# Kernel tuning notes

Hardware: AMD Instinct MI355X
Metric: run time of the kernel (lower is better)

Reference implementation:

```python
import jax, jax.numpy as jnp
import numpy as np

IN_DIM = 768
ATT_DIM = 512
N_HEADS = 8
HEAD_DIM = ATT_DIM // N_HEADS


def setup_inputs() -> dict:
    key = jax.random.key(0)
    k1, k2, k3 = jax.random.split(key, 3)
    X = jax.random.normal(k1, (4, 2048, IN_DIM), dtype=jnp.float32)
    # qkv linear (no bias): weight [3*att_dim, in_dim], torch convention y = x W^T
    W_qkv = jax.random.normal(k2, (3 * ATT_DIM, IN_DIM), dtype=jnp.float32) * (1.0 / np.sqrt(IN_DIM))
    W_out = jax.random.normal(k3, (IN_DIM, ATT_DIM), dtype=jnp.float32) * (1.0 / np.sqrt(ATT_DIM))
    b_out = jnp.zeros((IN_DIM,), dtype=jnp.float32)
    return {"X": X, "W_qkv": W_qkv, "W_out": W_out, "b_out": b_out}


def reference(X, W_qkv, W_out, b_out):
    b, n, _ = X.shape
    QKV = jnp.einsum('bnf,cf->bnc', X, W_qkv)  # [b, n, 3*att_dim]
    # rearrange 'b n (p h d) -> p b h n d'
    QKV = QKV.reshape(b, n, 3, N_HEADS, HEAD_DIM).transpose(2, 0, 3, 1, 4)
    Q, K, V = QKV[0], QKV[1], QKV[2]  # each [b, h, n, d]
    scores = jnp.einsum('bhid,bhjd->bhij', Q, K) / np.sqrt(HEAD_DIM)
    A = jax.nn.softmax(scores, axis=-1)  # dropout p=0 -> identity
    Y = jnp.einsum('bhij,bhjd->bhid', A, V)
    Y = Y.transpose(0, 2, 1, 3).reshape(b, n, ATT_DIM)  # 'b h n d -> b n (h d)'
    return jnp.einsum('bna,oa->bno', Y, W_out) + b_out
```

## Files before the change

kernel.cpp:

```cpp
#include <hip/hip_runtime.h>

typedef __bf16 bf16;
typedef unsigned int u32;
typedef __attribute__((ext_vector_type(8))) __bf16 bf16x8;
typedef __attribute__((ext_vector_type(4))) __bf16 bf16x4;
typedef __attribute__((ext_vector_type(4))) float floatx4;

#define IN_DIM  768
#define ATT_DIM 512
#define NH      8
#define HD      64
#define BATCH   4
#define SEQ     2048
#define M_TOT   (BATCH*SEQ)
#define QKV_N   (3*ATT_DIM)

#define QSCALE 0.18033688011112042f

__device__ __forceinline__ void cp16(void* lds, const void* g) {
    __builtin_amdgcn_global_load_lds((const __attribute__((address_space(1))) u32*)g,
                                     (__attribute__((address_space(3))) u32*)lds, 16, 0, 0);
}
__device__ __forceinline__ const bf16* swz(const bf16* b, int row, int chunk) {
    return b + row * 64 + (((chunk) ^ (row & 7)) << 3);
}
__device__ __forceinline__ const bf16* swz128(const bf16* b, int row, int chunk) {
    return b + row * 128 + (((chunk) ^ (row & 15)) << 3);
}

#define N8_X  (M_TOT * IN_DIM / 8)
#define N8_WQ (QKV_N * IN_DIM / 8)
#define N8_WO (IN_DIM * ATT_DIM / 8)
#define N8_ALL (N8_X + N8_WQ + N8_WO)

__global__ __launch_bounds__(256) void cvt_all(const float* __restrict__ X,
                                               const float* __restrict__ Wq,
                                               const float* __restrict__ Wo,
                                               bf16* __restrict__ Xb,
                                               bf16* __restrict__ Wqb,
                                               bf16* __restrict__ Wob) {
    int i = blockIdx.x * 256 + threadIdx.x;
    const float* s; bf16* d; int off;
    if (i < N8_X)            { s = X;  d = Xb;  off = i; }
    else if (i < N8_X+N8_WQ) { s = Wq; d = Wqb; off = i - N8_X; }
    else                     { s = Wo; d = Wob; off = i - N8_X - N8_WQ; }
    const float4 a = ((const float4*)s)[2*off];
    const float4 b = ((const float4*)s)[2*off+1];
    bf16x8 o = {(bf16)a.x,(bf16)a.y,(bf16)a.z,(bf16)a.w,
                (bf16)b.x,(bf16)b.y,(bf16)b.z,(bf16)b.w};
    ((bf16x8*)d)[off] = o;
}

__global__ __launch_bounds__(256) void qkv_gemm(const bf16* __restrict__ Xb,
                                                const bf16* __restrict__ Wb,
                                                bf16* __restrict__ Q,
                                                bf16* __restrict__ Kv,
                                                bf16* __restrict__ VT) {
    __shared__ __align__(16) char smraw[34816];
    bf16* As = (bf16*)smraw;
    bf16* Bs = (bf16*)(smraw + 16384);

    const int tid  = threadIdx.x;
    const int bm0  = blockIdx.y * 128;
    const int bn0  = blockIdx.x * 128;
    const int wave = tid >> 6, lane = tid & 63;
    const int quad = lane >> 4, l15 = lane & 15;
    const int wm = (wave >> 1) * 64, wn = (wave & 1) * 64;
    const int r8 = lane >> 3, cc = (lane & 7) ^ r8;

    const bf16* ag = Xb + (size_t)(bm0 + wave * 32 + r8) * IN_DIM + cc * 8;
    const bf16* bg = Wb + (size_t)(bn0 + wave * 32 + r8) * IN_DIM + cc * 8;

    floatx4 acc[4][4];
#pragma unroll
    for (int i = 0; i < 4; ++i)
#pragma unroll
        for (int j = 0; j < 4; ++j) acc[i][j] = (floatx4){0.f, 0.f, 0.f, 0.f};

    for (int kt = 0; kt < IN_DIM / 64; ++kt) {
        __syncthreads();
#pragma unroll
        for (int it = 0; it < 4; ++it) {
            cp16(&As[(wave * 32 + it * 8) * 64], ag + it * (8 * IN_DIM) + kt * 64);
            cp16(&Bs[(wave * 32 + it * 8) * 64], bg + it * (8 * IN_DIM) + kt * 64);
        }
        __syncthreads();

        bf16x8 af[2][4], bfr[2][4];
#pragma unroll
        for (int kh = 0; kh < 2; ++kh)
#pragma unroll
            for (int i = 0; i < 4; ++i) {
                af[kh][i]  = *(const bf16x8*)swz(As, wm + i * 16 + l15, kh * 4 + quad);
                bfr[kh][i] = *(const bf16x8*)swz(Bs, wn + i * 16 + l15, kh * 4 + quad);
            }
#pragma unroll
        for (int kh = 0; kh < 2; ++kh)
#pragma unroll
            for (int i = 0; i < 4; ++i)
#pragma unroll
                for (int j = 0; j < 4; ++j)
                    acc[i][j] = __builtin_amdgcn_mfma_f32_16x16x32_bf16(af[kh][i], bfr[kh][j], acc[i][j], 0, 0, 0);
    }

    const int b = bm0 >> 11, nbase = bm0 & 2047;

    if (bn0 < 1024) {
#pragma unroll
        for (int i = 0; i < 4; ++i)
#pragma unroll
            for (int j = 0; j < 4; ++j)
#pragma unroll
                for (int r = 0; r < 4; ++r) {
                    const int row = bm0 + wm + i * 16 + quad * 4 + r;
                    const int col = bn0 + wn + j * 16 + l15;
                    const float v = acc[i][j][r];
                    const int rem = col & 511;
                    const int h = rem >> 6, d = rem & 63;
                    const int n = row & 2047;
                    const size_t idx = (((size_t)((row >> 11) * NH + h)) * SEQ + n) * HD + d;
                    if (col < 512) Q[idx]  = (bf16)(v * QSCALE);
                    else           Kv[idx] = (bf16)v;
                }
    } else {
        __syncthreads();
        bf16 (*Ts)[136] = (bf16(*)[136])smraw;
#pragma unroll
        for (int i = 0; i < 4; ++i)
#pragma unroll
            for (int j = 0; j < 4; ++j) {
                bf16x4 pk = {(bf16)acc[i][j][0], (bf16)acc[i][j][1],
                             (bf16)acc[i][j][2], (bf16)acc[i][j][3]};
                *(bf16x4*)&Ts[wn + j * 16 + l15][wm + i * 16 + quad * 4] = pk;
            }
        __syncthreads();
        const int cb = bn0 - 1024;
#pragma unroll
        for (int t2 = 0; t2 < 8; ++t2) {
            const int id = tid + t2 * 256;
            const int c = id >> 4, nc = (id & 15) * 8;
            const int col = cb + c;
            const int h = col >> 6, d = col & 63;
            *(bf16x8*)&VT[(((size_t)(b * NH + h)) * HD + d) * SEQ + nbase + nc] =
                *(const bf16x8*)&Ts[c][nc];
        }
    }
}

__global__ __launch_bounds__(256, 2) void attn(const bf16* __restrict__ Q,
                                               const bf16* __restrict__ K,
                                               const bf16* __restrict__ VT,
                                               bf16* __restrict__ Y) {
    __shared__ bf16 Ks[2][128 * 64];
    __shared__ bf16 VTs[2][64 * 128];
    __shared__ bf16 Ps[4][2][16 * 64];

    const int tid  = threadIdx.x;
    const int wave = tid >> 6, lane = tid & 63;
    const int quad = lane >> 4, l15 = lane & 15;
    const int bh = blockIdx.x;
    const int q0 = blockIdx.y * 128;
    const bf16* Qg = Q  + (size_t)bh * SEQ * HD;
    const bf16* Kg = K  + (size_t)bh * SEQ * HD;
    const bf16* Vg = VT + (size_t)bh * HD * SEQ;

    const int r8 = lane >> 3, cc = (lane & 7) ^ r8;
    const int r4 = lane >> 4;

    bf16x8 aq[2][2];
#pragma unroll
    for (int g = 0; g < 2; ++g) {
        const size_t qrow = (size_t)(q0 + wave * 32 + g * 16 + l15) * 64;
        aq[g][0] = *(const bf16x8*)&Qg[qrow + quad * 8];
        aq[g][1] = *(const bf16x8*)&Qg[qrow + 32 + quad * 8];
    }

    const bf16* kgw = Kg + (size_t)(wave * 32 + r8) * 64 + cc * 8;
    float l[2] = {0.f, 0.f};
    floatx4 o[2][4];
#pragma unroll
    for (int g = 0; g < 2; ++g)
#pragma unroll
        for (int db = 0; db < 4; ++db) o[g][db] = (floatx4){0.f, 0.f, 0.f, 0.f};

#pragma unroll
    for (int it = 0; it < 4; ++it)
        cp16(&Ks[0][(wave * 32 + it * 8) * 64], kgw + (size_t)it * 8 * 64);
#pragma unroll
    for (int it = 0; it < 4; ++it) {
        const int vrow = wave * 16 + it * 4 + r4;
        const int vcc = (lane & 15) ^ (vrow & 15);
        cp16(&VTs[0][(wave * 16 + it * 4) * 128],
             Vg + (size_t)vrow * 2048 + vcc * 8);
    }

    for (int kt = 0; kt < SEQ / 128; ++kt) {
        const int cur = kt & 1, nb = cur ^ 1;
        __syncthreads();
        if (kt < SEQ / 128 - 1) {
#pragma unroll
            for (int it = 0; it < 4; ++it)
                cp16(&Ks[nb][(wave * 32 + it * 8) * 64],
                     kgw + (size_t)(kt + 1) * 128 * 64 + (size_t)it * 8 * 64);
#pragma unroll
            for (int it = 0; it < 4; ++it) {
                const int vrow = wave * 16 + it * 4 + r4;
                const int vcc = (lane & 15) ^ (vrow & 15);
                cp16(&VTs[nb][(wave * 16 + it * 4) * 128],
                     Vg + (size_t)vrow * 2048 + (kt + 1) * 128 + vcc * 8);
            }
        }

#pragma unroll
        for (int s = 0; s < 2; ++s) {
#pragma unroll
            for (int t = 0; t < 4; ++t) {
                const int kr = s * 64 + t * 16 + l15;
                const bf16x8 k0 = *(const bf16x8*)swz(Ks[cur], kr, quad);
                const bf16x8 k1 = *(const bf16x8*)swz(Ks[cur], kr, 4 + quad);
                const int c = t * 2 + (quad >> 1);
                const int poff = l15 * 64 + ((c ^ (l15 & 7)) << 3) + ((quad & 1) << 2);
#pragma unroll
                for (int g = 0; g < 2; ++g) {
                    floatx4 z = (floatx4){0.f, 0.f, 0.f, 0.f};
                    z = __builtin_amdgcn_mfma_f32_16x16x32_bf16(k0, aq[g][0], z, 0, 0, 0);
                    z = __builtin_amdgcn_mfma_f32_16x16x32_bf16(k1, aq[g][1], z, 0, 0, 0);
                    const float p0 = __builtin_amdgcn_exp2f(z[0]);
                    const float p1 = __builtin_amdgcn_exp2f(z[1]);
                    const float p2 = __builtin_amdgcn_exp2f(z[2]);
                    const float p3 = __builtin_amdgcn_exp2f(z[3]);
                    l[g] += (p0 + p1) + (p2 + p3);
                    bf16x4 pk = {(bf16)p0, (bf16)p1, (bf16)p2, (bf16)p3};
                    *(bf16x4*)&Ps[wave][g][poff] = pk;
                }
            }
            bf16x8 pa[2][2];
#pragma unroll
            for (int g = 0; g < 2; ++g) {
                pa[g][0] = *(const bf16x8*)swz(&Ps[wave][g][0], l15, quad);
                pa[g][1] = *(const bf16x8*)swz(&Ps[wave][g][0], l15, 4 + quad);
            }
#pragma unroll
            for (int db = 0; db < 4; ++db) {
                const int vr = db * 16 + l15;
                const bf16x8 v0 = *(const bf16x8*)swz128(VTs[cur], vr, s * 8 + quad);
                const bf16x8 v1 = *(const bf16x8*)swz128(VTs[cur], vr, s * 8 + 4 + quad);
#pragma unroll
                for (int g = 0; g < 2; ++g) {
                    o[g][db] = __builtin_amdgcn_mfma_f32_16x16x32_bf16(pa[g][0], v0, o[g][db], 0, 0, 0);
                    o[g][db] = __builtin_amdgcn_mfma_f32_16x16x32_bf16(pa[g][1], v1, o[g][db], 0, 0, 0);
                }
            }
        }
    }

    const int b = bh >> 3, h = bh & 7;
#pragma unroll
    for (int g = 0; g < 2; ++g) {
        float lg = l[g];
        lg += __shfl_xor(lg, 16, 64);
        lg += __shfl_xor(lg, 32, 64);
        const float inv = 1.0f / lg;
        float linv[4];
#pragma unroll
        for (int r = 0; r < 4; ++r)
            linv[r] = __int_as_float(__builtin_amdgcn_ds_bpermute((quad * 4 + r) * 4,
                                                                  __float_as_int(inv)));
#pragma unroll
        for (int db = 0; db < 4; ++db)
#pragma unroll
            for (int r = 0; r < 4; ++r) {
                const int n = q0 + wave * 32 + g * 16 + quad * 4 + r;
                Y[((size_t)(b * SEQ + n)) * ATT_DIM + h * HD + db * 16 + l15] =
                    (bf16)(o[g][db][r] * linv[r]);
            }
    }
}

__global__ __launch_bounds__(256) void out_gemm(const bf16* __restrict__ Yb,
                                                const bf16* __restrict__ Wb,
                                                const float* __restrict__ bias,
                                                float* __restrict__ out) {
    __shared__ __align__(16) bf16 As[128 * 64];
    __shared__ __align__(16) bf16 Bs[128 * 64];

    const int tid  = threadIdx.x;
    const int bm0  = blockIdx.y * 128;
    const int bn0  = blockIdx.x * 128;
    const int wave = tid >> 6, lane = tid & 63;
    const int quad = lane >> 4, l15 = lane & 15;
    const int wm = (wave >> 1) * 64, wn = (wave & 1) * 64;
    const int r8 = lane >> 3, cc = (lane & 7) ^ r8;

    const bf16* ag = Yb + (size_t)(bm0 + wave * 32 + r8) * ATT_DIM + cc * 8;
    const bf16* bg = Wb + (size_t)(bn0 + wave * 32 + r8) * ATT_DIM + cc * 8;

    floatx4 acc[4][4];
#pragma unroll
    for (int i = 0; i < 4; ++i)
#pragma unroll
        for (int j = 0; j < 4; ++j) acc[i][j] = (floatx4){0.f, 0.f, 0.f, 0.f};

    for (int kt = 0; kt < ATT_DIM / 64; ++kt) {
        __syncthreads();
#pragma unroll
        for (int it = 0; it < 4; ++it) {
            cp16(&As[(wave * 32 + it * 8) * 64], ag + it * (8 * ATT_DIM) + kt * 64);
            cp16(&Bs[(wave * 32 + it * 8) * 64], bg + it * (8 * ATT_DIM) + kt * 64);
        }
        __syncthreads();

        bf16x8 af[2][4], bfr[2][4];
#pragma unroll
        for (int kh = 0; kh < 2; ++kh)
#pragma unroll
            for (int i = 0; i < 4; ++i) {
                af[kh][i]  = *(const bf16x8*)swz(As, wm + i * 16 + l15, kh * 4 + quad);
                bfr[kh][i] = *(const bf16x8*)swz(Bs, wn + i * 16 + l15, kh * 4 + quad);
            }
#pragma unroll
        for (int kh = 0; kh < 2; ++kh)
#pragma unroll
            for (int i = 0; i < 4; ++i)
#pragma unroll
                for (int j = 0; j < 4; ++j)
                    acc[i][j] = __builtin_amdgcn_mfma_f32_16x16x32_bf16(af[kh][i], bfr[kh][j], acc[i][j], 0, 0, 0);
    }

#pragma unroll
    for (int i = 0; i < 4; ++i)
#pragma unroll
        for (int j = 0; j < 4; ++j)
#pragma unroll
            for (int r = 0; r < 4; ++r) {
                const int row = bm0 + wm + i * 16 + quad * 4 + r;
                const int col = bn0 + wn + j * 16 + l15;
                out[(size_t)row * IN_DIM + col] = acc[i][j][r] + bias[col];
            }
}

extern "C" void kernel_launch(void* const* d_in, const int* in_sizes, int n_in,
                              void* d_out, int out_size, void* d_ws, size_t ws_size,
                              hipStream_t stream) {
    const float* X    = (const float*)d_in[0];
    const float* Wqkv = (const float*)d_in[1];
    const float* Wout = (const float*)d_in[2];
    const float* bout = (const float*)d_in[3];
    float* out = (float*)d_out;

    char* ws = (char*)d_ws;
    size_t off = 0;
    bf16* Xb  = (bf16*)(ws + off); off += (size_t)M_TOT * IN_DIM * 2;
    bf16* Wqb = (bf16*)(ws + off); off += (size_t)QKV_N * IN_DIM * 2;
    bf16* Wob = (bf16*)(ws + off); off += (size_t)IN_DIM * ATT_DIM * 2;
    const size_t T = (size_t)BATCH * NH * SEQ * HD * 2;
    bf16* Q  = (bf16*)(ws + off); off += T;
    bf16* K  = (bf16*)(ws + off); off += T;
    bf16* VT = (bf16*)(ws + off); off += T;
    bf16* Y  = (bf16*)(ws + off); off += T;

    cvt_all<<<N8_ALL / 256, 256, 0, stream>>>(X, Wqkv, Wout, Xb, Wqb, Wob);
    qkv_gemm<<<dim3(QKV_N / 128, M_TOT / 128), 256, 0, stream>>>(Xb, Wqb, Q, K, VT);
    attn<<<dim3(BATCH * NH, SEQ / 128), 256, 0, stream>>>(Q, K, VT, Y);
    out_gemm<<<dim3(IN_DIM / 128, M_TOT / 128), 256, 0, stream>>>(Y, Wob, bout, out);
}
```

Baseline: 170.6 us.

## Rewrite attention with 32x32x16 MFMA and register-resident P via permlane swap

The attention kernel moves from 16x16x32 MFMAs to 32x32x16 MFMAs, with each wave owning 32 query rows. The P matrix is now repacked in registers using v_cvt_pk_bf16 and v_permlane32_swap instead of a round trip through LDS. K/V tiles shrink to 64 keys, which cuts shared memory and raises the occupancy target to 4 blocks per CU. The aim is to remove LDS traffic and syncs for P and improve MFMA efficiency, at the cost of twice as many loop iterations and barriers.

Result: faster. 162.7 us (-4.6%).

```diff
diff --git a/kernel.cpp b/kernel.cpp
--- a/kernel.cpp
+++ b/kernel.cpp
@@ -5,6 +5,8 @@
 typedef __attribute__((ext_vector_type(8))) __bf16 bf16x8;
 typedef __attribute__((ext_vector_type(4))) __bf16 bf16x4;
 typedef __attribute__((ext_vector_type(4))) float floatx4;
+typedef __attribute__((ext_vector_type(16))) float floatx16;
+typedef __attribute__((ext_vector_type(4))) int int4v;
 
 #define IN_DIM  768
 #define ATT_DIM 512
@@ -26,6 +28,15 @@
 }
 __device__ __forceinline__ const bf16* swz128(const bf16* b, int row, int chunk) {
     return b + row * 128 + (((chunk) ^ (row & 15)) << 3);
+}
+
+__device__ __forceinline__ int cvtpk_bf16(float lo, float hi) {
+    int r;
+    asm("v_cvt_pk_bf16_f32 %0, %1, %2" : "=v"(r) : "v"(lo), "v"(hi));
+    return r;
+}
+__device__ __forceinline__ void plswap(int& a, int& b) {
+    asm("v_permlane32_swap_b32 %0, %1" : "+v"(a), "+v"(b));
 }
 
 #define N8_X  (M_TOT * IN_DIM / 8)
@@ -147,133 +158,111 @@
     }
 }
 
-__global__ __launch_bounds__(256, 2) void attn(const bf16* __restrict__ Q,
+__global__ __launch_bounds__(256, 4) void attn(const bf16* __restrict__ Q,
                                                const bf16* __restrict__ K,
                                                const bf16* __restrict__ VT,
                                                bf16* __restrict__ Y) {
-    __shared__ bf16 Ks[2][128 * 64];
-    __shared__ bf16 VTs[2][64 * 128];
-    __shared__ bf16 Ps[4][2][16 * 64];
+    __shared__ bf16 Ks[2][64 * 64];
+    __shared__ bf16 VTs[2][64 * 64];
 
     const int tid  = threadIdx.x;
     const int wave = tid >> 6, lane = tid & 63;
-    const int quad = lane >> 4, l15 = lane & 15;
+    const int l31  = lane & 31, hi = lane >> 5;
     const int bh = blockIdx.x;
     const int q0 = blockIdx.y * 128;
     const bf16* Qg = Q  + (size_t)bh * SEQ * HD;
     const bf16* Kg = K  + (size_t)bh * SEQ * HD;
     const bf16* Vg = VT + (size_t)bh * HD * SEQ;
 
-    const int r8 = lane >> 3, cc = (lane & 7) ^ r8;
-    const int r4 = lane >> 4;
-
-    bf16x8 aq[2][2];
-#pragma unroll
-    for (int g = 0; g < 2; ++g) {
-        const size_t qrow = (size_t)(q0 + wave * 32 + g * 16 + l15) * 64;
-        aq[g][0] = *(const bf16x8*)&Qg[qrow + quad * 8];
-        aq[g][1] = *(const bf16x8*)&Qg[qrow + 32 + quad * 8];
-    }
-
-    const bf16* kgw = Kg + (size_t)(wave * 32 + r8) * 64 + cc * 8;
-    float l[2] = {0.f, 0.f};
-    floatx4 o[2][4];
-#pragma unroll
-    for (int g = 0; g < 2; ++g)
-#pragma unroll
-        for (int db = 0; db < 4; ++db) o[g][db] = (floatx4){0.f, 0.f, 0.f, 0.f};
-
-#pragma unroll
-    for (int it = 0; it < 4; ++it)
-        cp16(&Ks[0][(wave * 32 + it * 8) * 64], kgw + (size_t)it * 8 * 64);
-#pragma unroll
-    for (int it = 0; it < 4; ++it) {
-        const int vrow = wave * 16 + it * 4 + r4;
-        const int vcc = (lane & 15) ^ (vrow & 15);
-        cp16(&VTs[0][(wave * 16 + it * 4) * 128],
-             Vg + (size_t)vrow * 2048 + vcc * 8);
-    }
-
-    for (int kt = 0; kt < SEQ / 128; ++kt) {
-        const int cur = kt & 1, nb = cur ^ 1;
-        __syncthreads();
-        if (kt < SEQ / 128 - 1) {
-#pragma unroll
-            for (int it = 0; it < 4; ++it)
-                cp16(&Ks[nb][(wave * 32 + it * 8) * 64],
-                     kgw + (size_t)(kt + 1) * 128 * 64 + (size_t)it * 8 * 64);
-#pragma unroll
-            for (int it = 0; it < 4; ++it) {
-                const int vrow = wave * 16 + it * 4 + r4;
-                const int vcc = (lane & 15) ^ (vrow & 15);
-                cp16(&VTs[nb][(wave * 16 + it * 4) * 128],
-                     Vg + (size_t)vrow * 2048 + (kt + 1) * 128 + vcc * 8);
-            }
-        }
-
-#pragma unroll
-        for (int s = 0; s < 2; ++s) {
-#pragma unroll
-            for (int t = 0; t < 4; ++t) {
-                const int kr = s * 64 + t * 16 + l15;
-                const bf16x8 k0 = *(const bf16x8*)swz(Ks[cur], kr, quad);
-                const bf16x8 k1 = *(const bf16x8*)swz(Ks[cur], kr, 4 + quad);
-                const int c = t * 2 + (quad >> 1);
-                const int poff = l15 * 64 + ((c ^ (l15 & 7)) << 3) + ((quad & 1) << 2);
-#pragma unroll
-                for (int g = 0; g < 2; ++g) {
-                    floatx4 z = (floatx4){0.f, 0.f, 0.f, 0.f};
-                    z = __builtin_amdgcn_mfma_f32_16x16x32_bf16(k0, aq[g][0], z, 0, 0, 0);
-                    z = __builtin_amdgcn_mfma_f32_16x16x32_bf16(k1, aq[g][1], z, 0, 0, 0);
-                    const float p0 = __builtin_amdgcn_exp2f(z[0]);
-                    const float p1 = __builtin_amdgcn_exp2f(z[1]);
-                    const float p2 = __builtin_amdgcn_exp2f(z[2]);
-                    const float p3 = __builtin_amdgcn_exp2f(z[3]);
-                    l[g] += (p0 + p1) + (p2 + p3);
-                    bf16x4 pk = {(bf16)p0, (bf16)p1, (bf16)p2, (bf16)p3};
-                    *(bf16x4*)&Ps[wave][g][poff] = pk;
-                }
-            }
-            bf16x8 pa[2][2];
-#pragma unroll
-            for (int g = 0; g < 2; ++g) {
-                pa[g][0] = *(const bf16x8*)swz(&Ps[wave][g][0], l15, quad);
-                pa[g][1] = *(const bf16x8*)swz(&Ps[wave][g][0], l15, 4 + quad);
-            }
-#pragma unroll
-            for (int db = 0; db < 4; ++db) {
-                const int vr = db * 16 + l15;
-                const bf16x8 v0 = *(const bf16x8*)swz128(VTs[cur], vr, s * 8 + quad);
-                const bf16x8 v1 = *(const bf16x8*)swz128(VTs[cur], vr, s * 8 + 4 + quad);
-#pragma unroll
-                for (int g = 0; g < 2; ++g) {
-                    o[g][db] = __builtin_amdgcn_mfma_f32_16x16x32_bf16(pa[g][0], v0, o[g][db], 0, 0, 0);
-                    o[g][db] = __builtin_amdgcn_mfma_f32_16x16x32_bf16(pa[g][1], v1, o[g][db], 0, 0, 0);
-                }
-            }
-        }
-    }
-
+    bf16x8 aq[4];
+    {
+        const bf16* qrow = Qg + (size_t)(q0 + wave * 32 + l31) * HD;
+#pragma unroll
+        for (int c = 0; c < 4; ++c)
+            aq[c] = *(const bf16x8*)(qrow + c * 16 + hi * 8);
+    }
+
+    const int r8 = lane >> 3, cc8 = (lane & 7) ^ r8;
+    const bf16* kgw = Kg + (size_t)(wave * 16 + r8) * HD + cc8 * 8;
+    const bf16* vgw = Vg + (size_t)(wave * 16 + r8) * SEQ + cc8 * 8;
+
+    float l = 0.f;
+    floatx16 o[2];
+#pragma unroll
+    for (int i = 0; i < 16; ++i) { o[0][i] = 0.f; o[1][i] = 0.f; }
+
+#pragma unroll
+    for (int it = 0; it < 2; ++it) {
+        cp16(&Ks[0][(wave * 16 + it * 8) * 64], kgw + (size_t)(it * 8) * HD);
+        cp16(&VTs[0][(wave * 16 + it * 8) * 64], vgw + (size_t)(it * 8) * SEQ);
+    }
+
+    for (int kt = 0; kt < SEQ / 64; ++kt) {
+        const int cur = kt & 1;
+        __syncthreads();
+        if (kt < SEQ / 64 - 1) {
+#pragma unroll
+            for (int it = 0; it < 2; ++it) {
+                cp16(&Ks[cur ^ 1][(wave * 16 + it * 8) * 64],
+                     kgw + (size_t)((kt + 1) * 64 + it * 8) * HD);
+                cp16(&VTs[cur ^ 1][(wave * 16 + it * 8) * 64],
+                     vgw + (size_t)(it * 8) * SEQ + (kt + 1) * 64);
+            }
+        }
+
+#pragma unroll
+        for (int kb = 0; kb < 2; ++kb) {
+            const int krow = kb * 32 + l31;
+            floatx16 s;
+#pragma unroll
+            for (int i = 0; i < 16; ++i) s[i] = 0.f;
+#pragma unroll
+            for (int c = 0; c < 4; ++c) {
+                const bf16x8 kf = *(const bf16x8*)swz(Ks[cur], krow, c * 2 + hi);
+                s = __builtin_amdgcn_mfma_f32_32x32x16_bf16(kf, aq[c], s, 0, 0, 0);
+            }
+            float p[16];
+#pragma unroll
+            for (int i = 0; i < 16; ++i) p[i] = __builtin_amdgcn_exp2f(s[i]);
+            {
+                const float t0 = (p[0] + p[1]) + (p[2] + p[3]);
+                const float t1 = (p[4] + p[5]) + (p[6] + p[7]);
+                const float t2 = (p[8] + p[9]) + (p[10] + p[11]);
+                const float t3 = (p[12] + p[13]) + (p[14] + p[15]);
+                l += (t0 + t1) + (t2 + t3);
+            }
+            int w[8];
+#pragma unroll
+            for (int i = 0; i < 8; ++i) w[i] = cvtpk_bf16(p[2 * i], p[2 * i + 1]);
+            plswap(w[0], w[2]); plswap(w[1], w[3]);
+            plswap(w[4], w[6]); plswap(w[5], w[7]);
+            const int4v f0i = {w[0], w[1], w[2], w[3]};
+            const int4v f1i = {w[4], w[5], w[6], w[7]};
+            const bf16x8 f0 = __builtin_bit_cast(bf16x8, f0i);
+            const bf16x8 f1 = __builtin_bit_cast(bf16x8, f1i);
+#pragma unroll
+            for (int db = 0; db < 2; ++db) {
+                const int vrow = db * 32 + l31;
+                const bf16x8 v0 = *(const bf16x8*)swz(VTs[cur], vrow, kb * 4 + hi);
+                const bf16x8 v1 = *(const bf16x8*)swz(VTs[cur], vrow, kb * 4 + 2 + hi);
+                o[db] = __builtin_amdgcn_mfma_f32_32x32x16_bf16(f0, v0, o[db], 0, 0, 0);
+                o[db] = __builtin_amdgcn_mfma_f32_32x32x16_bf16(f1, v1, o[db], 0, 0, 0);
+            }
+        }
+    }
+
+    l += __shfl_xor(l, 32, 64);
+    const float inv = 1.0f / l;
     const int b = bh >> 3, h = bh & 7;
 #pragma unroll
-    for (int g = 0; g < 2; ++g) {
-        float lg = l[g];
-        lg += __shfl_xor(lg, 16, 64);
-        lg += __shfl_xor(lg, 32, 64);
-        const float inv = 1.0f / lg;
-        float linv[4];
-#pragma unroll
-        for (int r = 0; r < 4; ++r)
-            linv[r] = __int_as_float(__builtin_amdgcn_ds_bpermute((quad * 4 + r) * 4,
-                                                                  __float_as_int(inv)));
-#pragma unroll
-        for (int db = 0; db < 4; ++db)
-#pragma unroll
-            for (int r = 0; r < 4; ++r) {
-                const int n = q0 + wave * 32 + g * 16 + quad * 4 + r;
-                Y[((size_t)(b * SEQ + n)) * ATT_DIM + h * HD + db * 16 + l15] =
-                    (bf16)(o[g][db][r] * linv[r]);
-            }
+    for (int reg = 0; reg < 16; ++reg) {
+        const int qr = (reg & 3) + 8 * (reg >> 2) + 4 * hi;
+        const float li = __int_as_float(
+            __builtin_amdgcn_ds_bpermute(qr << 2, __float_as_int(inv)));
+        const int n = q0 + wave * 32 + qr;
+        bf16* yrow = Y + ((size_t)(b * SEQ + n)) * ATT_DIM + h * HD + l31;
+        yrow[0]  = (bf16)(o[0][reg] * li);
+        yrow[32] = (bf16)(o[1][reg] * li);
     }
 }
 
```
